# Kernel optimization log

Hardware: AMD Instinct MI355X
Metric: run time of the kernel (lower is better)

The kernel has to match this reference:

```python
import jax, jax.numpy as jnp
import numpy as np

B, H, LQ, LK, D = 2, 16, 2048, 2048, 128

def setup_inputs() -> dict:
    key = jax.random.key(0)
    k1, k2, k3 = jax.random.split(key, 3)
    q = jax.random.normal(k1, (B, H, LQ, D), dtype=jnp.float32)
    k = jax.random.normal(k2, (B, H, LK, D), dtype=jnp.float32)
    v = jax.random.normal(k3, (B, H, LK, D), dtype=jnp.float32)
    return {"q": q, "k": k, "v": v}

def reference(q, k, v):
    # scaled dot-product attention: softmax(q k^T / sqrt(D)) v
    scale = q.shape[-1] ** (-0.5)
    # scores: [B,H,Lq,Lk]
    scores = jnp.einsum('bhqd,bhkd->bhqk', q, k) * scale
    attn = jax.nn.softmax(scores, axis=-1)
    out = jnp.einsum('bhqk,bhkd->bhqd', attn, v)  # [B,H,Lq,Dv]
    return out
```

## Files before the change

kernel.cpp:

```cpp
#include <hip/hip_runtime.h>
#include <hip/hip_bf16.h>
#include <cstdint>

#define LQ_N   2048
#define LK_N   2048
#define DD     128
#define NHEADS 32
#define QBLK   256
#define KVBLK  64
#define NKV    (LK_N / KVBLK)
#define NQB    (LQ_N / QBLK)
#define SCALE  0.08838834764831845f
#define SCALE2 0.1275525003267101f

#define KTILE_BYTES (KVBLK * DD * 2)
#define WS_K_BYTES  ((size_t)NHEADS * NKV * KTILE_BYTES)
#define WS_NEED     (2 * WS_K_BYTES)

#define RING       4
#define SMEM_MAIN  (2 * RING * KTILE_BYTES)

#define PSTR 72

typedef __attribute__((ext_vector_type(8)))  short bf16x8;
typedef __attribute__((ext_vector_type(4)))  float f32x4;
typedef __attribute__((ext_vector_type(16))) float f32x16;

#if __has_builtin(__builtin_amdgcn_exp2f)
#define EXP2F __builtin_amdgcn_exp2f
#else
#define EXP2F exp2f
#endif

#define MFMA32(a, b, c) __builtin_amdgcn_mfma_f32_32x32x16_bf16((a), (b), (c), 0, 0, 0)
#define WAITV(N) asm volatile("s_waitcnt vmcnt(" #N ")" ::: "memory")

__device__ inline unsigned short f2bf(float f) {
    union { float f; unsigned u; } x; x.f = f;
    unsigned r = (x.u + 0x7fffu + ((x.u >> 16) & 1u)) >> 16;
    return (unsigned short)r;
}

__device__ inline unsigned cvt_pk_bf16(float lo, float hi) {
    unsigned r;
    asm("v_cvt_pk_bf16_f32 %0, %1, %2" : "=v"(r) : "v"(lo), "v"(hi));
    return r;
}

__device__ inline float fmax4(float a, float b, float c, float d) {
    return fmaxf(fmaxf(a, b), fmaxf(c, d));
}

__device__ inline bf16x8 make_pfrag(float v0, float v1, float v2, float v3,
                                    float v4, float v5, float v6, float v7) {
    unsigned a0 = cvt_pk_bf16(v0, v1);
    unsigned a1 = cvt_pk_bf16(v2, v3);
    unsigned b0 = cvt_pk_bf16(v4, v5);
    unsigned b1 = cvt_pk_bf16(v6, v7);
    asm("v_permlane32_swap_b32 %0, %1" : "+v"(a0), "+v"(b0));
    asm("v_permlane32_swap_b32 %0, %1" : "+v"(a1), "+v"(b1));
    union { unsigned u[4]; bf16x8 v8; } u;
    u.u[0] = a0; u.u[1] = a1; u.u[2] = b0; u.u[3] = b1;
    return u.v8;
}

__device__ inline void gld16(const char* g, const char* l) {
    __builtin_amdgcn_global_load_lds(
        (const __attribute__((address_space(1))) unsigned int*)g,
        (__attribute__((address_space(3))) unsigned int*)l,
        16, 0, 0);
}

__global__ __launch_bounds__(256, 2)
void prep_k_kernel(const float* __restrict__ K, char* __restrict__ ws)
{
    __shared__ unsigned short kt[KVBLK * 136];
    const int tid  = threadIdx.x;
    const int kvt  = blockIdx.x;
    const int head = blockIdx.y;
    const float* Kh = K + ((size_t)head * LK_N + (size_t)kvt * KVBLK) * DD;
    #pragma unroll
    for (int i = 0; i < 4; ++i) {
        int c = tid + 256 * i;
        int r  = c >> 4;
        int c8 = c & 15;
        const float* src = Kh + (size_t)r * DD + c8 * 8;
        float4 a = *(const float4*)src;
        float4 b = *(const float4*)(src + 4);
        bf16x8 t;
        t[0] = (short)f2bf(a.x * SCALE2); t[1] = (short)f2bf(a.y * SCALE2);
        t[2] = (short)f2bf(a.z * SCALE2); t[3] = (short)f2bf(a.w * SCALE2);
        t[4] = (short)f2bf(b.x * SCALE2); t[5] = (short)f2bf(b.y * SCALE2);
        t[6] = (short)f2bf(b.z * SCALE2); t[7] = (short)f2bf(b.w * SCALE2);
        *(bf16x8*)&kt[r * 136 + c8 * 8] = t;
    }
    __syncthreads();
    char* dst = ws + ((size_t)head * NKV + kvt) * KTILE_BYTES;
    #pragma unroll
    for (int i = 0; i < 4; ++i) {
        int c = tid + 256 * i;
        int g = c >> 6;
        int r = c & 63;
        bf16x8 t = *(const bf16x8*)&kt[r * 136 + g * 8];
        *(bf16x8*)(dst + c * 16) = t;
    }
}

__global__ __launch_bounds__(256, 2)
void prep_vt_kernel(const float* __restrict__ V, char* __restrict__ ws)
{
    __shared__ unsigned short vt[DD * PSTR];
    const int tid  = threadIdx.x;
    const int kvt  = blockIdx.x;
    const int head = blockIdx.y;
    const float* Vh = V + ((size_t)head * LK_N + (size_t)kvt * KVBLK) * DD;
    #pragma unroll
    for (int i = 0; i < 8; ++i) {
        int f = tid + 256 * i;
        int r  = f >> 5;
        int c4 = f & 31;
        float4 x = *(const float4*)(Vh + (size_t)r * DD + c4 * 4);
        vt[(c4 * 4 + 0) * PSTR + r] = f2bf(x.x);
        vt[(c4 * 4 + 1) * PSTR + r] = f2bf(x.y);
        vt[(c4 * 4 + 2) * PSTR + r] = f2bf(x.z);
        vt[(c4 * 4 + 3) * PSTR + r] = f2bf(x.w);
    }
    __syncthreads();
    char* dst = ws + WS_K_BYTES + ((size_t)head * NKV + kvt) * KTILE_BYTES;
    #pragma unroll
    for (int i = 0; i < 4; ++i) {
        int c = tid + 256 * i;
        int g = c >> 7;
        int d = c & 127;
        bf16x8 t = *(const bf16x8*)&vt[d * PSTR + g * 8];
        *(bf16x8*)(dst + c * 16) = t;
    }
}

#define PV_ROUND(S, B, KS) { \
    float e0 = EXP2F(S[B + 0] - m_run), e1 = EXP2F(S[B + 1] - m_run); \
    float e2 = EXP2F(S[B + 2] - m_run), e3 = EXP2F(S[B + 3] - m_run); \
    float e4 = EXP2F(S[B + 4] - m_run), e5 = EXP2F(S[B + 5] - m_run); \
    float e6 = EXP2F(S[B + 6] - m_run), e7 = EXP2F(S[B + 7] - m_run); \
    sum += ((e0 + e1) + (e2 + e3)) + ((e4 + e5) + (e6 + e7)); \
    bf16x8 pf = make_pfrag(e0, e1, e2, e3, e4, e5, e6, e7); \
    bf16x8 vf0 = *(const bf16x8*)(vb + (((2 * (KS) + h) * 128 +  0 + l31) << 4)); \
    bf16x8 vf1 = *(const bf16x8*)(vb + (((2 * (KS) + h) * 128 + 32 + l31) << 4)); \
    bf16x8 vf2 = *(const bf16x8*)(vb + (((2 * (KS) + h) * 128 + 64 + l31) << 4)); \
    bf16x8 vf3 = *(const bf16x8*)(vb + (((2 * (KS) + h) * 128 + 96 + l31) << 4)); \
    __builtin_amdgcn_s_setprio(1); \
    o_acc[0] = MFMA32(vf0, pf, o_acc[0]); \
    o_acc[1] = MFMA32(vf1, pf, o_acc[1]); \
    o_acc[2] = MFMA32(vf2, pf, o_acc[2]); \
    o_acc[3] = MFMA32(vf3, pf, o_acc[3]); \
    __builtin_amdgcn_s_setprio(0); }

__global__ __launch_bounds__(512, 1)
void attn_main_kernel(const float* __restrict__ Q, const char* __restrict__ kws,
                      const char* __restrict__ vws, float* __restrict__ O)
{
    extern __shared__ char smem[];

    const int tid  = threadIdx.x;
    const int lane = tid & 63;
    const int wave = tid >> 6;
    const int l31  = lane & 31;
    const int h    = lane >> 5;

    const int bid  = blockIdx.x;
    const int sid  = (bid & 7) * (NQB * NHEADS / 8) + (bid >> 3);
    const int head = sid >> 3;
    const int qb   = sid & 7;

    const float* Qh = Q + (size_t)head * LQ_N * DD;
    float*       Oh = O + (size_t)head * LQ_N * DD;
    const char*  kt_g = kws + (size_t)head * NKV * KTILE_BYTES;
    const char*  vt_g = vws + (size_t)head * NKV * KTILE_BYTES;

    const int qrow = qb * QBLK + wave * 32 + l31;
    bf16x8 qf[8];
    {
        const float* qp = Qh + (size_t)qrow * DD + 8 * h;
        #pragma unroll
        for (int kd = 0; kd < 8; ++kd) {
            float4 a = *(const float4*)(qp + 16 * kd);
            float4 b = *(const float4*)(qp + 16 * kd + 4);
            bf16x8 t;
            t[0] = (short)f2bf(a.x); t[1] = (short)f2bf(a.y);
            t[2] = (short)f2bf(a.z); t[3] = (short)f2bf(a.w);
            t[4] = (short)f2bf(b.x); t[5] = (short)f2bf(b.y);
            t[6] = (short)f2bf(b.z); t[7] = (short)f2bf(b.w);
            qf[kd] = t;
        }
    }
    asm volatile("s_waitcnt vmcnt(0)" ::: "memory");

    f32x16 o_acc[4];
    #pragma unroll
    for (int nt = 0; nt < 4; ++nt)
        #pragma unroll
        for (int i = 0; i < 16; ++i) o_acc[nt][i] = 0.f;
    float m_run = -1e30f, l_run = 0.f;

    auto issue_t = [&](int t) {
        const char* ks = kt_g + (size_t)t * KTILE_BYTES;
        const char* vs = vt_g + (size_t)t * KTILE_BYTES;
        const char* kl = smem + (size_t)(t & 3) * KTILE_BYTES;
        const char* vl = smem + (size_t)(RING + (t & 3)) * KTILE_BYTES;
        #pragma unroll
        for (int i = 0; i < 2; ++i) {
            int off = (tid + 512 * i) * 16;
            gld16(ks + off, kl + off);
            gld16(vs + off, vl + off);
        }
    };

    auto process = [&](int t) {
        const char* kb = smem + (size_t)(t & 3) * KTILE_BYTES;
        const char* vb = smem + (size_t)(RING + (t & 3)) * KTILE_BYTES;

        f32x16 s0, s1;
        #pragma unroll
        for (int i = 0; i < 16; ++i) { s0[i] = 0.f; s1[i] = 0.f; }
        __builtin_amdgcn_s_setprio(1);
        #pragma unroll
        for (int kd = 0; kd < 8; ++kd) {
            bf16x8 kf0 = *(const bf16x8*)(kb + (((2 * kd + h) * 64 + l31) << 4));
            bf16x8 kf1 = *(const bf16x8*)(kb + (((2 * kd + h) * 64 + 32 + l31) << 4));
            s0 = MFMA32(kf0, qf[kd], s0);
            s1 = MFMA32(kf1, qf[kd], s1);
        }
        __builtin_amdgcn_s_setprio(0);

        float x0 = fmax4(s0[0],  s0[1],  s0[2],  s0[3]);
        float x1 = fmax4(s0[4],  s0[5],  s0[6],  s0[7]);
        float x2 = fmax4(s0[8],  s0[9],  s0[10], s0[11]);
        float x3 = fmax4(s0[12], s0[13], s0[14], s0[15]);
        float y0 = fmax4(s1[0],  s1[1],  s1[2],  s1[3]);
        float y1 = fmax4(s1[4],  s1[5],  s1[6],  s1[7]);
        float y2 = fmax4(s1[8],  s1[9],  s1[10], s1[11]);
        float y3 = fmax4(s1[12], s1[13], s1[14], s1[15]);
        float pm = fmaxf(fmaxf(fmaxf(x0, x1), fmaxf(x2, x3)),
                         fmaxf(fmaxf(y0, y1), fmaxf(y2, y3)));
        pm = fmaxf(pm, __shfl_xor(pm, 32));

        if (!__all(pm <= m_run + 8.0f)) {
            float mn = fmaxf(m_run, pm);
            float al = EXP2F(m_run - mn);
            m_run = mn;
            l_run *= al;
            #pragma unroll
            for (int nt = 0; nt < 4; ++nt)
                #pragma unroll
                for (int i = 0; i < 16; ++i) o_acc[nt][i] *= al;
        }

        float sum = 0.f;
        PV_ROUND(s0, 0, 0);
        PV_ROUND(s0, 8, 1);
        PV_ROUND(s1, 0, 2);
        PV_ROUND(s1, 8, 3);
        sum += __shfl_xor(sum, 32);
        l_run += sum;
    };

    issue_t(0);
    issue_t(1);

    for (int t = 0; t < NKV; ++t) {
        if (t < NKV - 1) WAITV(4);
        else             WAITV(0);
        __builtin_amdgcn_s_barrier();
        __builtin_amdgcn_sched_barrier(0);
        if (t + 2 < NKV) issue_t(t + 2);
        process(t);
    }

    float inv = 1.0f / l_run;
    float* op = Oh + (size_t)qrow * DD;
    #pragma unroll
    for (int nt = 0; nt < 4; ++nt)
        #pragma unroll
        for (int p = 0; p < 4; ++p) {
            int dbase = 32 * nt + 8 * p + 4 * h;
            float4 w;
            w.x = o_acc[nt][4 * p + 0] * inv;
            w.y = o_acc[nt][4 * p + 1] * inv;
            w.z = o_acc[nt][4 * p + 2] * inv;
            w.w = o_acc[nt][4 * p + 3] * inv;
            *(float4*)(op + dbase) = w;
        }
}

#define KSTRIDE  136
#define VTSTRIDE 40
#define FKV 32

__global__ __launch_bounds__(256, 2)
void attn_fwd_fallback(const float* __restrict__ Q, const float* __restrict__ K,
                       const float* __restrict__ V, float* __restrict__ O)
{
    __shared__ unsigned short k_lds[FKV * KSTRIDE];
    __shared__ unsigned short vt_lds[DD * VTSTRIDE];
    __shared__ unsigned short p_lds2[4 * 16 * VTSTRIDE];

    const int tid  = threadIdx.x;
    const int lane = tid & 63;
    const int wave = tid >> 6;
    const int head = blockIdx.y;
    const int qb   = blockIdx.x;

    const float* Qh = Q + (size_t)head * LQ_N * DD;
    const float* Kh = K + (size_t)head * LK_N * DD;
    const float* Vh = V + (size_t)head * LK_N * DD;
    float*       Oh = O + (size_t)head * LQ_N * DD;

    const int r16 = lane & 15;
    const int g   = lane >> 4;

    const int qrow = qb * 64 + wave * 16 + r16;
    bf16x8 qf[4];
    {
        const float* qp = Qh + (size_t)qrow * DD + 8 * g;
        #pragma unroll
        for (int kt = 0; kt < 4; ++kt) {
            float4 a = *(const float4*)(qp + 32 * kt);
            float4 b = *(const float4*)(qp + 32 * kt + 4);
            bf16x8 t;
            t[0] = (short)f2bf(a.x * SCALE); t[1] = (short)f2bf(a.y * SCALE);
            t[2] = (short)f2bf(a.z * SCALE); t[3] = (short)f2bf(a.w * SCALE);
            t[4] = (short)f2bf(b.x * SCALE); t[5] = (short)f2bf(b.y * SCALE);
            t[6] = (short)f2bf(b.z * SCALE); t[7] = (short)f2bf(b.w * SCALE);
            qf[kt] = t;
        }
    }

    f32x4 o_acc[8];
    #pragma unroll
    for (int dt = 0; dt < 8; ++dt) o_acc[dt] = (f32x4){0.f, 0.f, 0.f, 0.f};
    float m_run[4], l_run[4];
    #pragma unroll
    for (int r = 0; r < 4; ++r) { m_run[r] = -1e30f; l_run[r] = 0.f; }

    for (int kv = 0; kv < LK_N / FKV; ++kv) {
        const float* Kt = Kh + (size_t)kv * FKV * DD;
        const float* Vt = Vh + (size_t)kv * FKV * DD;
        __syncthreads();
        #pragma unroll
        for (int i = 0; i < 4; ++i) {
            int f = tid + 256 * i;
            int row = f >> 5, colf = f & 31;
            float4 x = *(const float4*)(Kt + (size_t)row * DD + colf * 4);
            ushort4 pk;
            pk.x = f2bf(x.x); pk.y = f2bf(x.y); pk.z = f2bf(x.z); pk.w = f2bf(x.w);
            *(ushort4*)(&k_lds[row * KSTRIDE + colf * 4]) = pk;
        }
        #pragma unroll
        for (int i = 0; i < 4; ++i) {
            int f = tid + 256 * i;
            int row = f >> 5, colf = f & 31;
            float4 x = *(const float4*)(Vt + (size_t)row * DD + colf * 4);
            vt_lds[(colf * 4 + 0) * VTSTRIDE + row] = f2bf(x.x);
            vt_lds[(colf * 4 + 1) * VTSTRIDE + row] = f2bf(x.y);
            vt_lds[(colf * 4 + 2) * VTSTRIDE + row] = f2bf(x.z);
            vt_lds[(colf * 4 + 3) * VTSTRIDE + row] = f2bf(x.w);
        }
        __syncthreads();

        f32x4 s0 = (f32x4){0.f,0.f,0.f,0.f};
        f32x4 s1 = (f32x4){0.f,0.f,0.f,0.f};
        #pragma unroll
        for (int kt = 0; kt < 4; ++kt) {
            bf16x8 kf0 = *(const bf16x8*)&k_lds[(r16)      * KSTRIDE + 32 * kt + 8 * g];
            bf16x8 kf1 = *(const bf16x8*)&k_lds[(16 + r16) * KSTRIDE + 32 * kt + 8 * g];
            s0 = __builtin_amdgcn_mfma_f32_16x16x32_bf16(qf[kt], kf0, s0, 0, 0, 0);
            s1 = __builtin_amdgcn_mfma_f32_16x16x32_bf16(qf[kt], kf1, s1, 0, 0, 0);
        }

        float alpha[4];
        f32x4 p0, p1;
        #pragma unroll
        for (int r = 0; r < 4; ++r) {
            float t = fmaxf(s0[r], s1[r]);
            t = fmaxf(t, __shfl_xor(t, 1));
            t = fmaxf(t, __shfl_xor(t, 2));
            t = fmaxf(t, __shfl_xor(t, 4));
            t = fmaxf(t, __shfl_xor(t, 8));
            float mn = fmaxf(m_run[r], t);
            alpha[r] = __expf(m_run[r] - mn);
            m_run[r] = mn;
            p0[r] = __expf(s0[r] - mn);
            p1[r] = __expf(s1[r] - mn);
            float su = p0[r] + p1[r];
            su += __shfl_xor(su, 1);
            su += __shfl_xor(su, 2);
            su += __shfl_xor(su, 4);
            su += __shfl_xor(su, 8);
            l_run[r] = l_run[r] * alpha[r] + su;
        }

        unsigned short* pw = &p_lds2[wave * 16 * VTSTRIDE];
        #pragma unroll
        for (int r = 0; r < 4; ++r) {
            int row = 4 * g + r;
            pw[row * VTSTRIDE + r16]      = f2bf(p0[r]);
            pw[row * VTSTRIDE + 16 + r16] = f2bf(p1[r]);
        }
        bf16x8 pf = *(const bf16x8*)&pw[r16 * VTSTRIDE + 8 * g];

        #pragma unroll
        for (int dt = 0; dt < 8; ++dt) {
            #pragma unroll
            for (int r = 0; r < 4; ++r) o_acc[dt][r] *= alpha[r];
        }
        #pragma unroll
        for (int dt = 0; dt < 8; ++dt) {
            bf16x8 vf = *(const bf16x8*)&vt_lds[(16 * dt + r16) * VTSTRIDE + 8 * g];
            o_acc[dt] = __builtin_amdgcn_mfma_f32_16x16x32_bf16(pf, vf, o_acc[dt], 0, 0, 0);
        }
    }

    #pragma unroll
    for (int r = 0; r < 4; ++r) {
        float inv = 1.0f / l_run[r];
        int row = qb * 64 + wave * 16 + 4 * g + r;
        float* op = Oh + (size_t)row * DD + r16;
        #pragma unroll
        for (int dt = 0; dt < 8; ++dt)
            op[16 * dt] = o_acc[dt][r] * inv;
    }
}

extern "C" void kernel_launch(void* const* d_in, const int* in_sizes, int n_in,
                              void* d_out, int out_size, void* d_ws, size_t ws_size,
                              hipStream_t stream) {
    const float* q = (const float*)d_in[0];
    const float* k = (const float*)d_in[1];
    const float* v = (const float*)d_in[2];
    float* o = (float*)d_out;

    hipError_t attr_ok = hipFuncSetAttribute(
        (const void*)attn_main_kernel,
        hipFuncAttributeMaxDynamicSharedMemorySize, SMEM_MAIN);

    if (ws_size >= WS_NEED && attr_ok == hipSuccess) {
        char* ws = (char*)d_ws;
        prep_k_kernel <<<dim3(NKV, NHEADS), 256, 0, stream>>>(k, ws);
        prep_vt_kernel<<<dim3(NKV, NHEADS), 256, 0, stream>>>(v, ws);
        attn_main_kernel<<<dim3(NQB * NHEADS), 512, SMEM_MAIN, stream>>>(
            q, ws, ws + WS_K_BYTES, o);
    } else {
        attn_fwd_fallback<<<dim3(LQ_N / 64, NHEADS), 256, 0, stream>>>(q, k, v, o);
    }
}
```

Baseline: 98.64 us.

## Compute softmax row sum via MFMA with ones and prefetch V fragments early

Replaces the per-lane VALU summation and cross-half shuffle of the softmax denominator with an extra MFMA that multiplies a ones vector by the probability fragment, accumulating the row sum in a matrix accumulator. V fragments are now loaded from LDS in a double-buffered fashion ahead of the exp/max work, so LDS latency overlaps with the softmax arithmetic. The change adds one MFMA per round, 16 more accumulator registers, and 16 more for the extra V fragments, which raises register pressure. The rows' sums also now come from bf16-rounded probabilities, matching the values used in the PV product.

```diff
diff --git a/kernel.cpp b/kernel.cpp
--- a/kernel.cpp
+++ b/kernel.cpp
@@ -137,22 +137,24 @@
     }
 }
 
-#define PV_ROUND(S, B, KS) { \
+#define LOADVF(a0, a1, a2, a3, VB, KS) { \
+    a0 = *(const bf16x8*)((VB) + (((2 * (KS) + h) * 128 +  0 + l31) << 4)); \
+    a1 = *(const bf16x8*)((VB) + (((2 * (KS) + h) * 128 + 32 + l31) << 4)); \
+    a2 = *(const bf16x8*)((VB) + (((2 * (KS) + h) * 128 + 64 + l31) << 4)); \
+    a3 = *(const bf16x8*)((VB) + (((2 * (KS) + h) * 128 + 96 + l31) << 4)); }
+
+#define PV_ROUND(S, B, r0, r1, r2, r3) { \
     float e0 = EXP2F(S[B + 0] - m_run), e1 = EXP2F(S[B + 1] - m_run); \
     float e2 = EXP2F(S[B + 2] - m_run), e3 = EXP2F(S[B + 3] - m_run); \
     float e4 = EXP2F(S[B + 4] - m_run), e5 = EXP2F(S[B + 5] - m_run); \
     float e6 = EXP2F(S[B + 6] - m_run), e7 = EXP2F(S[B + 7] - m_run); \
-    sum += ((e0 + e1) + (e2 + e3)) + ((e4 + e5) + (e6 + e7)); \
     bf16x8 pf = make_pfrag(e0, e1, e2, e3, e4, e5, e6, e7); \
-    bf16x8 vf0 = *(const bf16x8*)(vb + (((2 * (KS) + h) * 128 +  0 + l31) << 4)); \
-    bf16x8 vf1 = *(const bf16x8*)(vb + (((2 * (KS) + h) * 128 + 32 + l31) << 4)); \
-    bf16x8 vf2 = *(const bf16x8*)(vb + (((2 * (KS) + h) * 128 + 64 + l31) << 4)); \
-    bf16x8 vf3 = *(const bf16x8*)(vb + (((2 * (KS) + h) * 128 + 96 + l31) << 4)); \
     __builtin_amdgcn_s_setprio(1); \
-    o_acc[0] = MFMA32(vf0, pf, o_acc[0]); \
-    o_acc[1] = MFMA32(vf1, pf, o_acc[1]); \
-    o_acc[2] = MFMA32(vf2, pf, o_acc[2]); \
-    o_acc[3] = MFMA32(vf3, pf, o_acc[3]); \
+    o_l      = MFMA32(ones8, pf, o_l); \
+    o_acc[0] = MFMA32(r0, pf, o_acc[0]); \
+    o_acc[1] = MFMA32(r1, pf, o_acc[1]); \
+    o_acc[2] = MFMA32(r2, pf, o_acc[2]); \
+    o_acc[3] = MFMA32(r3, pf, o_acc[3]); \
     __builtin_amdgcn_s_setprio(0); }
 
 __global__ __launch_bounds__(512, 1)
@@ -195,12 +197,18 @@
     }
     asm volatile("s_waitcnt vmcnt(0)" ::: "memory");
 
-    f32x16 o_acc[4];
+    bf16x8 ones8;
+    #pragma unroll
+    for (int i = 0; i < 8; ++i) ones8[i] = (short)0x3F80;
+
+    f32x16 o_acc[4], o_l;
     #pragma unroll
     for (int nt = 0; nt < 4; ++nt)
         #pragma unroll
         for (int i = 0; i < 16; ++i) o_acc[nt][i] = 0.f;
-    float m_run = -1e30f, l_run = 0.f;
+    #pragma unroll
+    for (int i = 0; i < 16; ++i) o_l[i] = 0.f;
+    float m_run = -1e30f;
 
     auto issue_t = [&](int t) {
         const char* ks = kt_g + (size_t)t * KTILE_BYTES;
@@ -217,7 +225,7 @@
 
     auto process = [&](int t) {
         const char* kb = smem + (size_t)(t & 3) * KTILE_BYTES;
-        const char* vb = smem + (size_t)(RING + (t & 3)) * KTILE_BYTES;
+        const char* vbase = smem + (size_t)(RING + (t & 3)) * KTILE_BYTES;
 
         f32x16 s0, s1;
         #pragma unroll
@@ -231,6 +239,10 @@
             s1 = MFMA32(kf1, qf[kd], s1);
         }
         __builtin_amdgcn_s_setprio(0);
+
+        bf16x8 va0, va1, va2, va3, vb0, vb1, vb2, vb3;
+        LOADVF(va0, va1, va2, va3, vbase, 0);
+        LOADVF(vb0, vb1, vb2, vb3, vbase, 1);
 
         float x0 = fmax4(s0[0],  s0[1],  s0[2],  s0[3]);
         float x1 = fmax4(s0[4],  s0[5],  s0[6],  s0[7]);
@@ -248,20 +260,20 @@
             float mn = fmaxf(m_run, pm);
             float al = EXP2F(m_run - mn);
             m_run = mn;
-            l_run *= al;
             #pragma unroll
             for (int nt = 0; nt < 4; ++nt)
                 #pragma unroll
                 for (int i = 0; i < 16; ++i) o_acc[nt][i] *= al;
-        }
-
-        float sum = 0.f;
-        PV_ROUND(s0, 0, 0);
-        PV_ROUND(s0, 8, 1);
-        PV_ROUND(s1, 0, 2);
-        PV_ROUND(s1, 8, 3);
-        sum += __shfl_xor(sum, 32);
-        l_run += sum;
+            #pragma unroll
+            for (int i = 0; i < 16; ++i) o_l[i] *= al;
+        }
+
+        PV_ROUND(s0, 0, va0, va1, va2, va3);
+        LOADVF(va0, va1, va2, va3, vbase, 2);
+        PV_ROUND(s0, 8, vb0, vb1, vb2, vb3);
+        LOADVF(vb0, vb1, vb2, vb3, vbase, 3);
+        PV_ROUND(s1, 0, va0, va1, va2, va3);
+        PV_ROUND(s1, 8, vb0, vb1, vb2, vb3);
     };
 
     issue_t(0);
@@ -276,7 +288,7 @@
         process(t);
     }
 
-    float inv = 1.0f / l_run;
+    float inv = 1.0f / o_l[0];
     float* op = Oh + (size_t)qrow * DD;
     #pragma unroll
     for (int nt = 0; nt < 4; ++nt)
```

New measurement: 98.58 us, median of 2. Within noise of the previous version (-0.1%).
